# Kernel optimization log

Measured on AMD Instinct MI355X. Metric: run time of the kernel, lower is better.

Reference implementation:

```python
import jax, jax.numpy as jnp
import numpy as np

EPS = 1e-5
GROUPS = 16  # 2*channels // chgn = 128 // 8


def _dft(xr, xi, inverse=False):
    """Matmul-based DFT along the last axis. xi may be None (real input)."""
    N = xr.shape[-1]
    n = jnp.arange(N, dtype=xr.dtype)
    ang = (2.0 * np.pi / N) * (n[:, None] * n[None, :])
    c, s = jnp.cos(ang), jnp.sin(ang)
    if xi is None:
        xi = jnp.zeros_like(xr)
    if inverse:
        yr = (xr @ c - xi @ s) / N
        yi = (xi @ c + xr @ s) / N
    else:
        yr = xr @ c + xi @ s
        yi = xi @ c - xr @ s
    return yr, yi


def _rfft(x):
    w = x.shape[-1]
    yr, yi = _dft(x, None, False)                 # DFT along width
    yr, yi = yr[..., : w // 2 + 1], yi[..., : w // 2 + 1]
    yr, yi = jnp.swapaxes(yr, -1, -2), jnp.swapaxes(yi, -1, -2)
    yr, yi = _dft(yr, yi, False)                  # DFT along height
    return jnp.swapaxes(yr, -1, -2), jnp.swapaxes(yi, -1, -2)


def _irfft(xr, xi):
    yr, yi = jnp.swapaxes(xr, -1, -2), jnp.swapaxes(xi, -1, -2)
    yr, yi = _dft(yr, yi, True)                   # inverse DFT along height
    yr, yi = jnp.swapaxes(yr, -1, -2), jnp.swapaxes(yi, -1, -2)
    # hermitian reconstruction along width
    yr = jnp.concatenate([yr, jnp.flip(yr[..., 1:-1], axis=-1)], axis=-1)
    yi = jnp.concatenate([yi, -jnp.flip(yi[..., 1:-1], axis=-1)], axis=-1)
    yr, _ = _dft(yr, yi, True)                    # inverse DFT along width, keep real
    return yr


def _block(y, conv_w, conv_b, gn_gamma, gn_beta):
    # 1x1 conv
    y = jnp.einsum('bchw,oc->bohw', y, conv_w) + conv_b[None, :, None, None]
    B, C, H, W = y.shape
    yg = y.reshape(B, GROUPS, C // GROUPS, H, W)
    mu = yg.mean(axis=(2, 3, 4), keepdims=True)
    var = yg.var(axis=(2, 3, 4), keepdims=True)
    yg = (yg - mu) * jax.lax.rsqrt(var + EPS)
    y = yg.reshape(B, C, H, W) * gn_gamma[None, :, None, None] + gn_beta[None, :, None, None]
    return jax.nn.relu(y)  # dropout=0.0 -> identity


def _fu(x, conv_w, conv_b, gn_gamma, gn_beta):
    ch = x.shape[1]
    yr, yi = _rfft(x)
    y = jnp.concatenate([yr, yi], axis=1)
    y = _block(y, conv_w, conv_b, gn_gamma, gn_beta)
    return _irfft(y[:, :ch], y[:, ch:])


def setup_inputs() -> dict:
    key = jax.random.key(0)
    k1, k2 = jax.random.split(key)
    x = jax.random.normal(k1, (4, 64, 256, 256), dtype=jnp.float32)
    conv_w = jax.random.normal(k2, (128, 128), dtype=jnp.float32) * (1.0 / np.sqrt(128.0))
    conv_b = jnp.zeros((128,), dtype=jnp.float32)
    gn_gamma = jnp.ones((128,), dtype=jnp.float32)
    gn_beta = jnp.zeros((128,), dtype=jnp.float32)
    return {"x": x, "conv_w": conv_w, "conv_b": conv_b, "gn_gamma": gn_gamma, "gn_beta": gn_beta}


def reference(x, conv_w, conv_b, gn_gamma, gn_beta):
    h = x.shape[2]
    bot = _fu(x[:, :, :-1, :], conv_w, conv_b, gn_gamma, gn_beta)
    top = _fu(x[:, :, 1:, :], conv_w, conv_b, gn_gamma, gn_beta)
    return jnp.concatenate([bot[:, :, : h // 2, :], top[:, :, h // 2 - 1 :, :]], axis=2)
```

## Files before the change

### kernel.cpp

```cpp
#include <hip/hip_runtime.h>
#include <math.h>

#define TPB 256

typedef unsigned short us16;
typedef __bf16 bf16x8 __attribute__((ext_vector_type(8)));
typedef float f32x4 __attribute__((ext_vector_type(4)));

static const int B_ALL = 4;
static const int CH   = 64;
static const int HIN  = 256, WIN = 256;
static const int HH   = 255;
static const int WF   = 129;
static const int HWF  = HH * WF;
static const int SP   = WF * 256;
static const int KH   = 160;
static const int UZ   = 64 * WF;
static const int NBX  = 258;
#define GN_EPS 1e-5f

__device__ __forceinline__ us16 f2bf(float f) {
  union { float f; unsigned u; } v; v.f = f;
  unsigned r = v.u + 0x7FFFu + ((v.u >> 16) & 1u);
  return (us16)(r >> 16);
}
__device__ __forceinline__ float bf2f(us16 v) {
  union { unsigned u; float f; } t; t.u = ((unsigned)v) << 16; return t.f;
}
__device__ __forceinline__ void gload16(const void* g, void* l) {
  __builtin_amdgcn_global_load_lds(
      (const __attribute__((address_space(1))) unsigned int*)g,
      (__attribute__((address_space(3))) unsigned int*)l, 16, 0, 0);
}
#define MFMA __builtin_amdgcn_mfma_f32_16x16x32_bf16
#define WAITVM(N) asm volatile("s_waitcnt vmcnt(" #N ")" ::: "memory")
#define BAR_ACQ() do { \
    __builtin_amdgcn_s_barrier(); \
    asm volatile("" ::: "memory"); \
    __builtin_amdgcn_sched_barrier(0); } while (0)
#define BAR_REL() do { \
    asm volatile("" ::: "memory"); \
    __builtin_amdgcn_s_barrier(); } while (0)

__global__ __launch_bounds__(TPB) void k_zero(float* __restrict__ out, int n) {
  int i = blockIdx.x * TPB + threadIdx.x;
  if (i < n) out[i] = 0.f;
}

__global__ __launch_bounds__(TPB) void k_xcast2(const float* __restrict__ x,
                                                us16* __restrict__ xb,
                                                us16* __restrict__ Frt,
                                                us16* __restrict__ Fit) {
  const int row = blockIdx.x * 4 + (threadIdx.x >> 6);
  const int lane = threadIdx.x & 63;
  float4 v = ((const float4*)(x + (size_t)row * 256))[lane];
  ushort4 o;
  o.x = f2bf(v.x); o.y = f2bf(v.y); o.z = f2bf(v.z); o.w = f2bf(v.w);
  ((ushort4*)(xb + (size_t)row * 256))[lane] = o;
  float alt = v.x - v.y + v.z - v.w;
  for (int off = 32; off; off >>= 1) alt += __shfl_down(alt, off);
  if (lane == 0) {
    int bc = row >> 8, h = row & 255;
    size_t idx = ((size_t)bc * WF + 128) * 256 + h;
    Frt[idx] = f2bf(alt);
    Fit[idx] = 0;
  }
}

__global__ __launch_bounds__(TPB) void k_tables(
    us16* __restrict__ CbA, us16* __restrict__ SbA,
    us16* __restrict__ Tcb, us16* __restrict__ Tsb,
    us16* __restrict__ Tci, us16* __restrict__ Tsi,
    us16* __restrict__ Wpb, us16* __restrict__ Wqb,
    const float* __restrict__ conv_w) {
  int i = blockIdx.x * TPB + threadIdx.x;
  const double PI2 = 6.283185307179586476925286766559;
  if (i < 2 * 65536) {
    int fu = i >> 16, r = (i >> 8) & 255, k = i & 255;
    float cv = 0.f, sv = 0.f;
    int kk = k - fu;
    if (r < 255 && kk >= 0 && kk < 255) {
      double ang = PI2 * (double)((r * kk) % 255) / 255.0;
      cv = (float)cos(ang); sv = (float)sin(ang);
    }
    CbA[i] = f2bf(cv); SbA[i] = f2bf(sv);
  }
  if (i < 128 * 256) {
    int n = i >> 8, w = i & 255;
    double ang = PI2 * (double)((n * w) & 255) / 256.0;
    Tcb[i] = f2bf((float)cos(ang));
    Tsb[i] = f2bf((float)sin(ang));
  }
  if (i < 256 * KH) {
    int w = i / KH, k = i - w * KH;
    float cv = 0.f, sv = 0.f;
    if (k < WF) {
      double coef = (k == 0 || k == 128) ? 1.0 : 2.0;
      double ang = PI2 * (double)((k * w) & 255) / 256.0;
      cv = (float)(coef * cos(ang) / 256.0);
      sv = (float)(coef * sin(ang) / 256.0);
    }
    Tci[i] = f2bf(cv); Tsi[i] = f2bf(sv);
  }
  if (i < 128 * 128) {
    int o = i >> 7, c = i & 127;
    Wpb[i] = f2bf(conv_w[i]);
    float q = (c < 64) ? -conv_w[o * 128 + 64 + c] : conv_w[o * 128 + c - 64];
    Wqb[i] = f2bf(q);
  }
}

__global__ __launch_bounds__(TPB) void k_dftw_fwd_mfma(
    const us16* __restrict__ xb, const us16* __restrict__ Tcb,
    const us16* __restrict__ Tsb, us16* __restrict__ Frt, us16* __restrict__ Fit) {
  __shared__ __align__(16) us16 Ac[2][2][64][32];
  __shared__ __align__(16) us16 As[2][2][64][32];
  __shared__ __align__(16) us16 Bx[2][64][32];
  const int tid = threadIdx.x, w = tid >> 6, lane = tid & 63;
  const int hb = blockIdx.x;
  const int rsel = lane >> 2;
  const int csw = (lane & 3) ^ ((lane >> 3) & 3);
  const us16* gAc = Tcb + (size_t)(16 * w + rsel) * 256 + csw * 8;
  const us16* gAs = Tsb + (size_t)(16 * w + rsel) * 256 + csw * 8;
  const us16* gB  = xb + ((size_t)hb * 64 + 16 * w + rsel) * 256 + csw * 8;
  f32x4 accr[2][4] = {}, acci[2][4] = {};
  const int fr = lane & 15;
  const int kb = 8 * ((lane >> 4) ^ ((lane >> 1) & 3));
#define STAGE_K1(pp, k0) do { \
    gload16(gAc + (k0), &Ac[pp][0][16 * w][0]); \
    gload16(gAc + 64 * 256 + (k0), &Ac[pp][1][16 * w][0]); \
    gload16(gAs + (k0), &As[pp][0][16 * w][0]); \
    gload16(gAs + 64 * 256 + (k0), &As[pp][1][16 * w][0]); \
    gload16(gB + (k0), &Bx[pp][16 * w][0]); } while (0)
  STAGE_K1(0, 0);
  int pp = 0;
  for (int k0 = 0; k0 < 256; k0 += 32) {
    if (k0 + 32 < 256) { STAGE_K1(pp ^ 1, k0 + 32); WAITVM(5); }
    else WAITVM(0);
    BAR_ACQ();
    bf16x8 aC[2], aSn[2];
#pragma unroll
    for (int g = 0; g < 2; ++g) {
      aC[g] = *(const bf16x8*)&Ac[pp][g][16 * w + fr][kb];
      bf16x8 aS = *(const bf16x8*)&As[pp][g][16 * w + fr][kb];
      uint4 su = *(const uint4*)&aS;
      su.x ^= 0x80008000u; su.y ^= 0x80008000u; su.z ^= 0x80008000u; su.w ^= 0x80008000u;
      aSn[g] = *(const bf16x8*)&su;
    }
#pragma unroll
    for (int t = 0; t < 4; ++t) {
      bf16x8 b = *(const bf16x8*)&Bx[pp][16 * t + fr][kb];
#pragma unroll
      for (int g = 0; g < 2; ++g) {
        accr[g][t] = MFMA(aC[g], b, accr[g][t], 0, 0, 0);
        acci[g][t] = MFMA(aSn[g], b, acci[g][t], 0, 0, 0);
      }
    }
    BAR_REL();
    pp ^= 1;
  }
  const int bc = hb >> 2, hl = (hb & 3) * 64;
#pragma unroll
  for (int g = 0; g < 2; ++g) {
#pragma unroll
    for (int t = 0; t < 4; ++t) {
      int h = hl + 16 * t + fr;
#pragma unroll
      for (int j = 0; j < 4; ++j) {
        int n = g * 64 + 16 * w + 4 * (lane >> 4) + j;
        size_t idx = ((size_t)bc * WF + n) * 256 + h;
        Frt[idx] = f2bf(accr[g][t][j]);
        Fit[idx] = f2bf(acci[g][t][j]);
      }
    }
  }
}

__global__ __launch_bounds__(TPB) void k_mix(
    const us16* __restrict__ Frt, const us16* __restrict__ Fit,
    const us16* __restrict__ Wpb, const us16* __restrict__ Wqb,
    us16* __restrict__ P, us16* __restrict__ Q) {
  __shared__ __align__(16) us16 Ap[2][64][32];
  __shared__ __align__(16) us16 Aq[2][64][32];
  __shared__ __align__(8)  us16 Bs[64][36];
  const int tid = threadIdx.x, w = tid >> 6, lane = tid & 63;
  const int sp0 = blockIdx.x * 64, b = blockIdx.z;
  const int rsel = lane >> 2;
  const int csw = (lane & 3) ^ ((lane >> 3) & 3);
  const us16* gAp0 = Wpb + (size_t)(16 * w + rsel) * 128 + csw * 8;
  const us16* gAq0 = Wqb + (size_t)(16 * w + rsel) * 128 + csw * 8;
  f32x4 accp[2][4] = {}, accq[2][4] = {};
  const int fr = lane & 15;
  const int kbA = 8 * ((lane >> 4) ^ ((lane >> 1) & 3));
  const int kbB = 8 * (lane >> 4);
  for (int c0 = 0; c0 < 128; c0 += 32) {
    gload16(gAp0 + c0, &Ap[0][16 * w][0]);
    gload16(gAp0 + 64 * 128 + c0, &Ap[1][16 * w][0]);
    gload16(gAq0 + c0, &Aq[0][16 * w][0]);
    gload16(gAq0 + 64 * 128 + c0, &Aq[1][16 * w][0]);
    for (int f = tid; f < 1024; f += TPB) {
      int cl = f >> 5, spp = f & 31;
      int c = c0 + cl;
      const us16* src = (c < 64) ? Frt : Fit;
      size_t addr = (size_t)(b * 64 + (c & 63)) * SP + sp0 + 2 * spp;
      unsigned v = *(const unsigned*)(src + addr);
      Bs[2 * spp][cl] = (us16)v;
      Bs[2 * spp + 1][cl] = (us16)(v >> 16);
    }
    __syncthreads();
    bf16x8 aP0 = *(const bf16x8*)&Ap[0][16 * w + fr][kbA];
    bf16x8 aP1 = *(const bf16x8*)&Ap[1][16 * w + fr][kbA];
    bf16x8 aQ0 = *(const bf16x8*)&Aq[0][16 * w + fr][kbA];
    bf16x8 aQ1 = *(const bf16x8*)&Aq[1][16 * w + fr][kbA];
#pragma unroll
    for (int t = 0; t < 4; ++t) {
      uint2 lo = *(const uint2*)&Bs[16 * t + fr][kbB];
      uint2 hi = *(const uint2*)&Bs[16 * t + fr][kbB + 4];
      uint4 qq; qq.x = lo.x; qq.y = lo.y; qq.z = hi.x; qq.w = hi.y;
      bf16x8 bb = *(const bf16x8*)&qq;
      accp[0][t] = MFMA(aP0, bb, accp[0][t], 0, 0, 0);
      accp[1][t] = MFMA(aP1, bb, accp[1][t], 0, 0, 0);
      accq[0][t] = MFMA(aQ0, bb, accq[0][t], 0, 0, 0);
      accq[1][t] = MFMA(aQ1, bb, accq[1][t], 0, 0, 0);
    }
    __syncthreads();
  }
#pragma unroll
  for (int t = 0; t < 4; ++t) {
    int sp = sp0 + 16 * t + fr;
#pragma unroll
    for (int ot = 0; ot < 2; ++ot)
#pragma unroll
      for (int j = 0; j < 4; ++j) {
        int o = ot * 64 + 16 * w + 4 * (lane >> 4) + j;
        size_t idx = (size_t)(b * 128 + o) * SP + sp;
        P[idx] = f2bf(accp[ot][t][j]);
        Q[idx] = f2bf(accq[ot][t][j]);
      }
  }
}

__global__ __launch_bounds__(TPB) void k_dfth_fwd2(
    const us16* __restrict__ P, const us16* __restrict__ Q,
    const us16* __restrict__ CbA, const us16* __restrict__ SbA,
    const float* __restrict__ bias, us16* __restrict__ Yt,
    float* __restrict__ gnpart, int fu) {
  __shared__ __align__(16) us16 Ac[2][2][64][32];
  __shared__ __align__(16) us16 As[2][2][64][32];
  __shared__ __align__(16) us16 Bp[2][64][32];
  __shared__ __align__(16) us16 Bq[2][64][32];
  __shared__ float red[4 * TPB];
  const int tid = threadIdx.x, w = tid >> 6, lane = tid & 63;
  const int b = blockIdx.z;
  const int u0 = blockIdx.x * 64;
  const int rsel = lane >> 2;
  const int csw = (lane & 3) ^ ((lane >> 3) & 3);
  const us16* gAc = CbA + (((size_t)fu * 256 + 16 * w + rsel) << 8) + csw * 8;
  const us16* gAs = SbA + (((size_t)fu * 256 + 16 * w + rsel) << 8) + csw * 8;
  const us16* gBp = P + (size_t)b * 128 * SP + (size_t)(u0 + 16 * w + rsel) * 256 + csw * 8;
  const us16* gBq = Q + (size_t)b * 128 * SP + (size_t)(u0 + 16 * w + rsel) * 256 + csw * 8;
  f32x4 cp[2][4] = {}, sq[2][4] = {};
  const int fr = lane & 15;
  const int kb = 8 * ((lane >> 4) ^ ((lane >> 1) & 3));
#define STAGE_K3(pp, k0) do { \
    _Pragma("unroll") \
    for (int mt = 0; mt < 2; ++mt) { \
      gload16(gAc + (mt << 14) + (k0), &Ac[pp][mt][16 * w][0]); \
      gload16(gAs + (mt << 14) + (k0), &As[pp][mt][16 * w][0]); } \
    gload16(gBp + (k0), &Bp[pp][16 * w][0]); \
    gload16(gBq + (k0), &Bq[pp][16 * w][0]); } while (0)
  STAGE_K3(0, 0);
  int pp = 0;
  for (int k0 = 0; k0 < 256; k0 += 32) {
    if (k0 + 32 < 256) { STAGE_K3(pp ^ 1, k0 + 32); WAITVM(6); }
    else WAITVM(0);
    BAR_ACQ();
    bf16x8 aC[2], aS[2];
#pragma unroll
    for (int mt = 0; mt < 2; ++mt) {
      aC[mt] = *(const bf16x8*)&Ac[pp][mt][16 * w + fr][kb];
      aS[mt] = *(const bf16x8*)&As[pp][mt][16 * w + fr][kb];
    }
#pragma unroll
    for (int t = 0; t < 4; ++t) {
      bf16x8 bP = *(const bf16x8*)&Bp[pp][16 * t + fr][kb];
      bf16x8 bQ = *(const bf16x8*)&Bq[pp][16 * t + fr][kb];
#pragma unroll
      for (int mt = 0; mt < 2; ++mt) {
        cp[mt][t] = MFMA(aC[mt], bP, cp[mt][t], 0, 0, 0);
        sq[mt][t] = MFMA(aS[mt], bQ, sq[mt][t], 0, 0, 0);
      }
    }
    BAR_REL();
    pp ^= 1;
  }
  us16* yb = Yt + (size_t)b * 128 * SP;
  const int mb_ = 16 * w + 4 * (lane >> 4);
  const int ub = (u0 / WF + 1) * WF;
  float s0 = 0.f, q0 = 0.f, s1 = 0.f, q1 = 0.f;
#pragma unroll
  for (int t = 0; t < 4; ++t) {
    int u = u0 + 16 * t + fr;
    float bo = bias[u / WF];
    float ts = 0.f, tq = 0.f;
#pragma unroll
    for (int mt = 0; mt < 2; ++mt) {
      int base = mt * 64 + mb_;
      float y[4], z[4];
#pragma unroll
      for (int j = 0; j < 4; ++j) {
        y[j] = cp[mt][t][j] + sq[mt][t][j] + bo;
        z[j] = cp[mt][t][j] - sq[mt][t][j] + bo;
        ts += y[j]; tq += y[j] * y[j];
        if (base + j) { ts += z[j]; tq += z[j] * z[j]; }
      }
      uint2 pk;
      pk.x = (unsigned)f2bf(y[0]) | ((unsigned)f2bf(y[1]) << 16);
      pk.y = (unsigned)f2bf(y[2]) | ((unsigned)f2bf(y[3]) << 16);
      *(uint2*)(yb + (size_t)u * 256 + base) = pk;
      uint2 pk2;
      pk2.x = (unsigned)f2bf(z[3]) | ((unsigned)f2bf(z[2]) << 16);
      pk2.y = (unsigned)f2bf(z[1]) | ((unsigned)f2bf(z[0]) << 16);
      *(uint2*)(yb + (size_t)u * 256 + 252 - base) = pk2;
    }
    if (u >= ub) { s1 += ts; q1 += tq; } else { s0 += ts; q0 += tq; }
  }
  __syncthreads();
  red[tid] = s0; red[TPB + tid] = q0;
  red[2 * TPB + tid] = s1; red[3 * TPB + tid] = q1;
  __syncthreads();
  for (int st = TPB / 2; st > 0; st >>= 1) {
    if (tid < st) {
      red[tid] += red[tid + st];
      red[TPB + tid] += red[TPB + tid + st];
      red[2 * TPB + tid] += red[2 * TPB + tid + st];
      red[3 * TPB + tid] += red[3 * TPB + tid + st];
    }
    __syncthreads();
  }
  if (tid == 0) {
    float* gp = gnpart + ((size_t)b * NBX + blockIdx.x) * 4;
    gp[0] = red[0]; gp[1] = red[TPB];
    gp[2] = red[2 * TPB]; gp[3] = red[3 * TPB];
  }
}

__global__ __launch_bounds__(TPB) void k_gn_stats2(const float* __restrict__ part,
                                                   float* __restrict__ stats) {
  const int bg = blockIdx.x, b = bg >> 4, g = bg & 15;
  const int tid = threadIdx.x;
  const int clo = g * 8, chi = clo + 8;
  float s = 0.f, ss = 0.f;
  for (int bx = tid; bx < NBX; bx += TPB) {
    int c0 = (bx * 64) / WF;
    int c1 = (bx * 64 + 63) / WF;
    const float* p = part + ((size_t)b * NBX + bx) * 4;
    if (c0 >= clo && c0 < chi) { s += p[0]; ss += p[1]; }
    if (c1 != c0 && c1 >= clo && c1 < chi) { s += p[2]; ss += p[3]; }
  }
  __shared__ float rs[TPB], rq[TPB];
  rs[tid] = s; rq[tid] = ss;
  __syncthreads();
  for (int st = TPB / 2; st > 0; st >>= 1) {
    if (tid < st) { rs[tid] += rs[tid + st]; rq[tid] += rq[tid + st]; }
    __syncthreads();
  }
  if (tid == 0) {
    const float inv = 1.f / (8.f * (float)HWF);
    float mean = rs[0] * inv;
    float var = rq[0] * inv - mean * mean;
    stats[bg * 2] = mean;
    stats[bg * 2 + 1] = rsqrtf(var + GN_EPS);
  }
}

__global__ __launch_bounds__(TPB) void k_gnfold(
    const us16* __restrict__ Yt, const float* __restrict__ stats,
    const float* __restrict__ gamma, const float* __restrict__ beta,
    us16* __restrict__ Zrp, us16* __restrict__ Zrm,
    us16* __restrict__ Zip, us16* __restrict__ Zim) {
  const int b = blockIdx.y;
  const int up = blockIdx.x * 8 + (threadIdx.x >> 5);
  const int l32 = threadIdx.x & 31;
  const int c = up / WF;
  const int g1 = b * 16 + (c >> 3), g2 = g1 + 8;
  const float sc1 = gamma[c] * stats[g1 * 2 + 1];
  const float sh1 = beta[c] - stats[g1 * 2] * sc1;
  const float sc2 = gamma[64 + c] * stats[g2 * 2 + 1];
  const float sh2 = beta[64 + c] - stats[g2 * 2] * sc2;
  const us16* ybase = Yt + (size_t)b * 128 * SP;
  const us16* yr = ybase + (size_t)up * 256;
  const us16* yi = ybase + (size_t)(64 * WF + up) * 256;
  const int k0 = l32 * 4;
  uint2 ar = *(const uint2*)(yr + k0);
  uint2 mr = *(const uint2*)(yr + 252 - k0);
  uint2 ai = *(const uint2*)(yi + k0);
  uint2 mi = *(const uint2*)(yi + 252 - k0);
  us16 arv[4] = {(us16)ar.x, (us16)(ar.x >> 16), (us16)ar.y, (us16)(ar.y >> 16)};
  us16 mrv[4] = {(us16)mr.x, (us16)(mr.x >> 16), (us16)mr.y, (us16)(mr.y >> 16)};
  us16 aiv[4] = {(us16)ai.x, (us16)(ai.x >> 16), (us16)ai.y, (us16)(ai.y >> 16)};
  us16 miv[4] = {(us16)mi.x, (us16)(mi.x >> 16), (us16)mi.y, (us16)(mi.y >> 16)};
  us16 rp[4], rm[4], ip[4], im[4];
#pragma unroll
  for (int d = 0; d < 4; ++d) {
    float zr = fmaxf(bf2f(arv[d]) * sc1 + sh1, 0.f);
    float zi = fmaxf(bf2f(aiv[d]) * sc2 + sh2, 0.f);
    float pr = 0.f, pi = 0.f;
    if (k0 + d > 0) {
      pr = fmaxf(bf2f(mrv[3 - d]) * sc1 + sh1, 0.f);
      pi = fmaxf(bf2f(miv[3 - d]) * sc2 + sh2, 0.f);
    }
    rp[d] = f2bf(zr + pr); rm[d] = f2bf(zr - pr);
    ip[d] = f2bf(zi + pi); im[d] = f2bf(zi - pi);
  }
  const size_t zo = ((size_t)b * UZ + up) * 128 + k0;
  uint2 o1; o1.x = (unsigned)rp[0] | ((unsigned)rp[1] << 16);
  o1.y = (unsigned)rp[2] | ((unsigned)rp[3] << 16);
  *(uint2*)(Zrp + zo) = o1;
  uint2 o2; o2.x = (unsigned)rm[0] | ((unsigned)rm[1] << 16);
  o2.y = (unsigned)rm[2] | ((unsigned)rm[3] << 16);
  *(uint2*)(Zrm + zo) = o2;
  uint2 o3; o3.x = (unsigned)ip[0] | ((unsigned)ip[1] << 16);
  o3.y = (unsigned)ip[2] | ((unsigned)ip[3] << 16);
  *(uint2*)(Zip + zo) = o3;
  uint2 o4; o4.x = (unsigned)im[0] | ((unsigned)im[1] << 16);
  o4.y = (unsigned)im[2] | ((unsigned)im[3] << 16);
  *(uint2*)(Zim + zo) = o4;
}

__global__ __launch_bounds__(TPB) void k_dfth_inv_mfma(
    const us16* __restrict__ Zrp, const us16* __restrict__ Zrm,
    const us16* __restrict__ Zip, const us16* __restrict__ Zim,
    const us16* __restrict__ CbA, const us16* __restrict__ SbA,
    us16* __restrict__ Hr, us16* __restrict__ Hi, int hsel) {
  __shared__ __align__(16) us16 Ac[2][2][64][32];
  __shared__ __align__(16) us16 As[2][2][64][32];
  __shared__ __align__(16) us16 Brp[2][64][32];
  __shared__ __align__(16) us16 Brm[2][64][32];
  __shared__ __align__(16) us16 Bip[2][64][32];
  __shared__ __align__(16) us16 Bim[2][64][32];
  const int tid = threadIdx.x, w = tid >> 6, lane = tid & 63;
  const int b = blockIdx.z;
  const int u0 = blockIdx.x * 64;
  const int rsel = lane >> 2;
  const int csw = (lane & 3) ^ ((lane >> 3) & 3);
  const us16* gAc = CbA + (((size_t)hsel + 16 * w + rsel) << 8) + csw * 8;
  const us16* gAs = SbA + (((size_t)hsel + 16 * w + rsel) << 8) + csw * 8;
  const size_t zoff = ((size_t)b * UZ + u0 + 16 * w + rsel) * 128 + csw * 8;
  const us16* gZrp = Zrp + zoff;
  const us16* gZrm = Zrm + zoff;
  const us16* gZip = Zip + zoff;
  const us16* gZim = Zim + zoff;
  f32x4 accr[2][4] = {}, acci[2][4] = {};
  const int fr = lane & 15;
  const int kb = 8 * ((lane >> 4) ^ ((lane >> 1) & 3));
#define STAGE_K6(pp, k0) do { \
    gload16(gAc + (k0), &Ac[pp][0][16 * w][0]); \
    gload16(gAc + (1 << 14) + (k0), &Ac[pp][1][16 * w][0]); \
    gload16(gAs + (k0), &As[pp][0][16 * w][0]); \
    gload16(gAs + (1 << 14) + (k0), &As[pp][1][16 * w][0]); \
    gload16(gZrp + (k0), &Brp[pp][16 * w][0]); \
    gload16(gZrm + (k0), &Brm[pp][16 * w][0]); \
    gload16(gZip + (k0), &Bip[pp][16 * w][0]); \
    gload16(gZim + (k0), &Bim[pp][16 * w][0]); } while (0)
  STAGE_K6(0, 0);
  int pp = 0;
  for (int k0 = 0; k0 < 128; k0 += 32) {
    if (k0 + 32 < 128) { STAGE_K6(pp ^ 1, k0 + 32); WAITVM(8); }
    else WAITVM(0);
    BAR_ACQ();
    bf16x8 aC[2], aS[2], aSn[2];
#pragma unroll
    for (int mt = 0; mt < 2; ++mt) {
      aC[mt] = *(const bf16x8*)&Ac[pp][mt][16 * w + fr][kb];
      aS[mt] = *(const bf16x8*)&As[pp][mt][16 * w + fr][kb];
      uint4 su = *(const uint4*)&aS[mt];
      su.x ^= 0x80008000u; su.y ^= 0x80008000u; su.z ^= 0x80008000u; su.w ^= 0x80008000u;
      aSn[mt] = *(const bf16x8*)&su;
    }
#pragma unroll
    for (int t = 0; t < 4; ++t) {
      bf16x8 bRp = *(const bf16x8*)&Brp[pp][16 * t + fr][kb];
      bf16x8 bRm = *(const bf16x8*)&Brm[pp][16 * t + fr][kb];
      bf16x8 bIp = *(const bf16x8*)&Bip[pp][16 * t + fr][kb];
      bf16x8 bIm = *(const bf16x8*)&Bim[pp][16 * t + fr][kb];
#pragma unroll
      for (int mt = 0; mt < 2; ++mt) {
        accr[mt][t] = MFMA(aC[mt], bRp, accr[mt][t], 0, 0, 0);
        accr[mt][t] = MFMA(aSn[mt], bIm, accr[mt][t], 0, 0, 0);
        acci[mt][t] = MFMA(aC[mt], bIp, acci[mt][t], 0, 0, 0);
        acci[mt][t] = MFMA(aS[mt], bRm, acci[mt][t], 0, 0, 0);
      }
    }
    BAR_REL();
    pp ^= 1;
  }
  const float inv = 1.f / 255.f;
#pragma unroll
  for (int t = 0; t < 4; ++t) {
    int u = u0 + 16 * t + fr;
    int c = u / WF, n = u - c * WF;
#pragma unroll
    for (int mt = 0; mt < 2; ++mt) {
#pragma unroll
      for (int j = 0; j < 4; ++j) {
        int m = mt * 64 + 16 * w + 4 * (lane >> 4) + j;
        size_t idx = (((size_t)(b * 64 + c)) * 128 + m) * KH + n;
        Hr[idx] = f2bf(accr[mt][t][j] * inv);
        Hi[idx] = f2bf(acci[mt][t][j] * inv);
      }
    }
  }
}

__global__ __launch_bounds__(TPB) void k_dftw_inv_mfma(
    const us16* __restrict__ Hr, const us16* __restrict__ Hi,
    const us16* __restrict__ Tci, const us16* __restrict__ Tsi,
    float* __restrict__ out, int roff, int b0) {
  __shared__ __align__(16) us16 Ar[2][64][32];
  __shared__ __align__(16) us16 Ai[2][64][32];
  __shared__ __align__(16) us16 Bc[2][64][32];
  __shared__ __align__(16) us16 Bs[2][64][32];
  const int tid = threadIdx.x, w = tid >> 6, lane = tid & 63;
  const int w0 = blockIdx.x * 64, mf0 = blockIdx.y * 64;
  const int rsel = lane >> 2;
  const int csw = (lane & 3) ^ ((lane >> 3) & 3);
  const us16* gAr = Hr + (size_t)(mf0 + 16 * w + rsel) * KH + csw * 8;
  const us16* gAi = Hi + (size_t)(mf0 + 16 * w + rsel) * KH + csw * 8;
  const us16* gBc = Tci + (size_t)(w0 + 16 * w + rsel) * KH + csw * 8;
  const us16* gBs = Tsi + (size_t)(w0 + 16 * w + rsel) * KH + csw * 8;
  f32x4 accU[4] = {}, accV[4] = {};
  const int fr = lane & 15;
  const int kb = 8 * ((lane >> 4) ^ ((lane >> 1) & 3));
#define STAGE_K7(pp, k0) do { \
    gload16(gAr + (k0), &Ar[pp][16 * w][0]); \
    gload16(gAi + (k0), &Ai[pp][16 * w][0]); \
    gload16(gBc + (k0), &Bc[pp][16 * w][0]); \
    gload16(gBs + (k0), &Bs[pp][16 * w][0]); } while (0)
  STAGE_K7(0, 0);
  int pp = 0;
  for (int k0 = 0; k0 < KH; k0 += 32) {
    if (k0 + 32 < KH) { STAGE_K7(pp ^ 1, k0 + 32); WAITVM(4); }
    else WAITVM(0);
    BAR_ACQ();
    bf16x8 aR = *(const bf16x8*)&Ar[pp][16 * w + fr][kb];
    bf16x8 aI = *(const bf16x8*)&Ai[pp][16 * w + fr][kb];
    uint4 su = *(const uint4*)&aI;
    su.x ^= 0x80008000u; su.y ^= 0x80008000u; su.z ^= 0x80008000u; su.w ^= 0x80008000u;
    bf16x8 aIn = *(const bf16x8*)&su;
#pragma unroll
    for (int t = 0; t < 4; ++t) {
      bf16x8 bC = *(const bf16x8*)&Bc[pp][16 * t + fr][kb];
      bf16x8 bS = *(const bf16x8*)&Bs[pp][16 * t + fr][kb];
      accU[t] = MFMA(aR, bC, accU[t], 0, 0, 0);
      accV[t] = MFMA(aIn, bS, accV[t], 0, 0, 0);
    }
    BAR_REL();
    pp ^= 1;
  }
#pragma unroll
  for (int t = 0; t < 4; ++t) {
    int wv = w0 + 16 * t + fr;
#pragma unroll
    for (int j = 0; j < 4; ++j) {
      int mf = mf0 + 16 * w + 4 * (lane >> 4) + j;
      int bcl = mf >> 7, mrow = mf & 127;
      int bb = b0 + (bcl >> 6), cc = bcl & 63;
      size_t obase = (((size_t)bb * CH + cc) * HIN + roff + mrow) * WIN;
      float U = accU[t][j], V = accV[t][j];
      out[obase + wv] = U + V;
      if (wv > 0) out[obase + 256 - wv] = U - V;
    }
  }
}

__global__ __launch_bounds__(TPB) void k_w128(const us16* __restrict__ Hr,
                                              float* __restrict__ out,
                                              int roff, int b0) {
  const int mf = blockIdx.x * TPB + threadIdx.x;
  const us16* hr = Hr + (size_t)mf * KH;
  float s = bf2f(hr[0]) + bf2f(hr[128]);
  for (int k = 1; k < 128; k += 2)
    s += -2.f * bf2f(hr[k]) + 2.f * bf2f(hr[k + 1]);
  s -= 2.f * bf2f(hr[128]);
  s *= (1.f / 256.f);
  int bcl = mf >> 7, mrow = mf & 127;
  int bb = b0 + (bcl >> 6), cc = bcl & 63;
  out[(((size_t)bb * CH + cc) * HIN + roff + mrow) * WIN + 128] = s;
}

extern "C" void kernel_launch(void* const* d_in, const int* in_sizes, int n_in,
                              void* d_out, int out_size, void* d_ws, size_t ws_size,
                              hipStream_t stream) {
  const float* x        = (const float*)d_in[0];
  const float* conv_w   = (const float*)d_in[1];
  const float* conv_b   = (const float*)d_in[2];
  const float* gn_gamma = (const float*)d_in[3];
  const float* gn_beta  = (const float*)d_in[4];
  float* out = (float*)d_out;

  const size_t uCbA = 2 * 65536;
  const size_t uTcb = 128 * 256;
  const size_t uTci = (size_t)256 * KH;
  const size_t uW   = 128 * 128;
  const size_t fixed_u16 = 2 * uCbA + 2 * uTcb + 2 * uTci + 2 * uW;
  const size_t uXB = (size_t)CH * HIN * WIN;
  const size_t uF  = (size_t)CH * SP;
  const size_t uPQ = (size_t)128 * SP;
  const size_t uYT = (size_t)128 * SP;
  const size_t uH  = (size_t)CH * 128 * KH;
  const size_t uZ1 = (size_t)UZ * 128;
  const size_t per_u16 = uXB + 2 * uF + 2 * uPQ + 4 * uZ1;
  const size_t nPart = 4 * 4 * NBX + 128;

  int nb = 0;
  for (int cand = 4; cand >= 1; cand >>= 1) {
    size_t need = fixed_u16 * 2 + nPart * 4 + (size_t)cand * per_u16 * 2 + 256;
    if (need <= ws_size) { nb = cand; break; }
  }
  if (nb == 0) {
    k_zero<<<dim3((out_size + TPB - 1) / TPB), dim3(TPB), 0, stream>>>(out, out_size);
    return;
  }

  us16* CbA = (us16*)d_ws;
  us16* SbA = CbA + uCbA;
  us16* Tcb = SbA + uCbA;
  us16* Tsb = Tcb + uTcb;
  us16* Tci = Tsb + uTcb;
  us16* Tsi = Tci + uTci;
  us16* Wpb = Tsi + uTci;
  us16* Wqb = Wpb + uW;
  float* part  = (float*)(Wqb + uW);
  float* stats = part + 4 * NBX * 4;
  us16* xb  = (us16*)(stats + 128);
  us16* Frt = xb + (size_t)nb * uXB;
  us16* Fit = Frt + (size_t)nb * uF;
  us16* P   = Fit + (size_t)nb * uF;
  us16* Q   = P + (size_t)nb * uPQ;
  us16* Zrp = Q + (size_t)nb * uPQ;
  us16* Zrm = Zrp + (size_t)nb * uZ1;
  us16* Zip = Zrm + (size_t)nb * uZ1;
  us16* Zim = Zip + (size_t)nb * uZ1;
  us16* Yt  = xb;
  us16* Hr  = xb + (size_t)nb * uYT;
  us16* Hi  = Hr + (size_t)nb * uH;

  k_tables<<<dim3(512), dim3(TPB), 0, stream>>>(CbA, SbA, Tcb, Tsb, Tci, Tsi,
                                                Wpb, Wqb, conv_w);

  for (int b0 = 0; b0 < B_ALL; b0 += nb) {
    k_xcast2<<<dim3(nb * 4096), dim3(TPB), 0, stream>>>(
        x + (size_t)b0 * CH * HIN * WIN, xb, Frt, Fit);
    k_dftw_fwd_mfma<<<dim3(nb * 256), dim3(TPB), 0, stream>>>(
        xb, Tcb, Tsb, Frt, Fit);
    k_mix<<<dim3(SP / 64, 1, nb), dim3(TPB), 0, stream>>>(
        Frt, Fit, Wpb, Wqb, P, Q);
    for (int fu = 0; fu < 2; ++fu) {
      const int hsel = fu ? 127 : 0;
      const int roff = fu ? 128 : 0;
      k_dfth_fwd2<<<dim3(NBX, 1, nb), dim3(TPB), 0, stream>>>(
          P, Q, CbA, SbA, conv_b, Yt, part, fu);
      k_gn_stats2<<<dim3(nb * 16), dim3(TPB), 0, stream>>>(part, stats);
      k_gnfold<<<dim3(UZ / 8, nb), dim3(TPB), 0, stream>>>(
          Yt, stats, gn_gamma, gn_beta, Zrp, Zrm, Zip, Zim);
      k_dfth_inv_mfma<<<dim3(UZ / 64, 1, nb), dim3(TPB), 0, stream>>>(
          Zrp, Zrm, Zip, Zim, CbA, SbA, Hr, Hi, hsel);
      k_dftw_inv_mfma<<<dim3(2, nb * 128), dim3(TPB), 0, stream>>>(
          Hr, Hi, Tci, Tsi, out, roff, b0);
      k_w128<<<dim3(nb * 32), dim3(TPB), 0, stream>>>(Hr, out, roff, b0);
    }
  }
}
```

Measured before the change: 248.8 us.

## Compute both shifted-window forward height DFTs in one kernel via phase rotation

The two forward height-DFT launches (one per shifted window) are merged into one kernel. The second window's result comes from the first window's DFT sums by a per-frequency twiddle rotation plus a boundary-row correction, so the P/Q inputs and the DFT tables are read once instead of twice. In exchange the kernel runs twice as many MFMAs per tile (four accumulator sets instead of two), uses more registers, and writes both outputs, which needs an extra Yt buffer and duplicated GN partial sums. The rotation identity also changes rounding relative to computing the second window directly.

Result: slower. 260.1 us (+4.6%).

```diff
diff --git a/kernel.cpp b/kernel.cpp
--- a/kernel.cpp
+++ b/kernel.cpp
@@ -72,6 +72,7 @@
     us16* __restrict__ Tcb, us16* __restrict__ Tsb,
     us16* __restrict__ Tci, us16* __restrict__ Tsi,
     us16* __restrict__ Wpb, us16* __restrict__ Wqb,
+    float* __restrict__ rot,
     const float* __restrict__ conv_w) {
   int i = blockIdx.x * TPB + threadIdx.x;
   const double PI2 = 6.283185307179586476925286766559;
@@ -107,6 +108,11 @@
     Wpb[i] = f2bf(conv_w[i]);
     float q = (c < 64) ? -conv_w[o * 128 + 64 + c] : conv_w[o * 128 + c - 64];
     Wqb[i] = f2bf(q);
+  }
+  if (i < 128) {
+    double ang = PI2 * (double)i / 255.0;
+    rot[2 * i] = (float)cos(ang);
+    rot[2 * i + 1] = (float)sin(ang);
   }
 }
 
@@ -243,23 +249,23 @@
 __global__ __launch_bounds__(TPB) void k_dfth_fwd2(
     const us16* __restrict__ P, const us16* __restrict__ Q,
     const us16* __restrict__ CbA, const us16* __restrict__ SbA,
-    const float* __restrict__ bias, us16* __restrict__ Yt,
-    float* __restrict__ gnpart, int fu) {
+    const float* __restrict__ bias, const float* __restrict__ rot,
+    us16* __restrict__ Yt0, us16* __restrict__ Yt1,
+    float* __restrict__ gnpart) {
   __shared__ __align__(16) us16 Ac[2][2][64][32];
   __shared__ __align__(16) us16 As[2][2][64][32];
   __shared__ __align__(16) us16 Bp[2][64][32];
   __shared__ __align__(16) us16 Bq[2][64][32];
-  __shared__ float red[4 * TPB];
   const int tid = threadIdx.x, w = tid >> 6, lane = tid & 63;
   const int b = blockIdx.z;
   const int u0 = blockIdx.x * 64;
   const int rsel = lane >> 2;
   const int csw = (lane & 3) ^ ((lane >> 3) & 3);
-  const us16* gAc = CbA + (((size_t)fu * 256 + 16 * w + rsel) << 8) + csw * 8;
-  const us16* gAs = SbA + (((size_t)fu * 256 + 16 * w + rsel) << 8) + csw * 8;
+  const us16* gAc = CbA + (((size_t)(16 * w + rsel)) << 8) + csw * 8;
+  const us16* gAs = SbA + (((size_t)(16 * w + rsel)) << 8) + csw * 8;
   const us16* gBp = P + (size_t)b * 128 * SP + (size_t)(u0 + 16 * w + rsel) * 256 + csw * 8;
   const us16* gBq = Q + (size_t)b * 128 * SP + (size_t)(u0 + 16 * w + rsel) * 256 + csw * 8;
-  f32x4 cp[2][4] = {}, sq[2][4] = {};
+  f32x4 cp[2][4] = {}, sq[2][4] = {}, sp_[2][4] = {}, cq[2][4] = {};
   const int fr = lane & 15;
   const int kb = 8 * ((lane >> 4) ^ ((lane >> 1) & 3));
 #define STAGE_K3(pp, k0) do { \
@@ -287,61 +293,98 @@
       bf16x8 bQ = *(const bf16x8*)&Bq[pp][16 * t + fr][kb];
 #pragma unroll
       for (int mt = 0; mt < 2; ++mt) {
-        cp[mt][t] = MFMA(aC[mt], bP, cp[mt][t], 0, 0, 0);
-        sq[mt][t] = MFMA(aS[mt], bQ, sq[mt][t], 0, 0, 0);
+        cp[mt][t]  = MFMA(aC[mt], bP, cp[mt][t], 0, 0, 0);
+        sp_[mt][t] = MFMA(aS[mt], bP, sp_[mt][t], 0, 0, 0);
+        cq[mt][t]  = MFMA(aC[mt], bQ, cq[mt][t], 0, 0, 0);
+        sq[mt][t]  = MFMA(aS[mt], bQ, sq[mt][t], 0, 0, 0);
       }
     }
     BAR_REL();
     pp ^= 1;
   }
-  us16* yb = Yt + (size_t)b * 128 * SP;
+  us16* yb0 = Yt0 + (size_t)b * 128 * SP;
+  us16* yb1 = Yt1 + (size_t)b * 128 * SP;
+  const us16* pb = P + (size_t)b * 128 * SP;
+  const us16* qb = Q + (size_t)b * 128 * SP;
   const int mb_ = 16 * w + 4 * (lane >> 4);
   const int ub = (u0 / WF + 1) * WF;
-  float s0 = 0.f, q0 = 0.f, s1 = 0.f, q1 = 0.f;
+  float rc[2][4], rs[2][4];
+#pragma unroll
+  for (int mt = 0; mt < 2; ++mt)
+#pragma unroll
+    for (int j = 0; j < 4; ++j) {
+      int r = mt * 64 + mb_ + j;
+      rc[mt][j] = rot[2 * r];
+      rs[mt][j] = rot[2 * r + 1];
+    }
+  float s0f0 = 0.f, q0f0 = 0.f, s1f0 = 0.f, q1f0 = 0.f;
+  float s0f1 = 0.f, q0f1 = 0.f, s1f1 = 0.f, q1f1 = 0.f;
 #pragma unroll
   for (int t = 0; t < 4; ++t) {
     int u = u0 + 16 * t + fr;
     float bo = bias[u / WF];
-    float ts = 0.f, tq = 0.f;
+    float dP = bf2f(pb[(size_t)u * 256 + 255]) - bf2f(pb[(size_t)u * 256]);
+    float dQ = bf2f(qb[(size_t)u * 256 + 255]) - bf2f(qb[(size_t)u * 256]);
+    float t0s = 0.f, t0q = 0.f, t1s = 0.f, t1q = 0.f;
 #pragma unroll
     for (int mt = 0; mt < 2; ++mt) {
       int base = mt * 64 + mb_;
-      float y[4], z[4];
+      float y0[4], z0[4], y1[4], z1[4];
 #pragma unroll
       for (int j = 0; j < 4; ++j) {
-        y[j] = cp[mt][t][j] + sq[mt][t][j] + bo;
-        z[j] = cp[mt][t][j] - sq[mt][t][j] + bo;
-        ts += y[j]; tq += y[j] * y[j];
-        if (base + j) { ts += z[j]; tq += z[j] * z[j]; }
+        float CPv = cp[mt][t][j], SQv = sq[mt][t][j];
+        float SPv = sp_[mt][t][j], CQv = cq[mt][t][j];
+        y0[j] = CPv + SQv + bo;
+        z0[j] = CPv - SQv + bo;
+        float E1 = rc[mt][j] * (CPv + dP) + rs[mt][j] * SPv;
+        float O1 = rc[mt][j] * SQv - rs[mt][j] * (CQv + dQ);
+        y1[j] = E1 + O1 + bo;
+        z1[j] = E1 - O1 + bo;
+        t0s += y0[j]; t0q += y0[j] * y0[j];
+        t1s += y1[j]; t1q += y1[j] * y1[j];
+        if (base + j) {
+          t0s += z0[j]; t0q += z0[j] * z0[j];
+          t1s += z1[j]; t1q += z1[j] * z1[j];
+        }
       }
       uint2 pk;
-      pk.x = (unsigned)f2bf(y[0]) | ((unsigned)f2bf(y[1]) << 16);
-      pk.y = (unsigned)f2bf(y[2]) | ((unsigned)f2bf(y[3]) << 16);
-      *(uint2*)(yb + (size_t)u * 256 + base) = pk;
-      uint2 pk2;
-      pk2.x = (unsigned)f2bf(z[3]) | ((unsigned)f2bf(z[2]) << 16);
-      pk2.y = (unsigned)f2bf(z[1]) | ((unsigned)f2bf(z[0]) << 16);
-      *(uint2*)(yb + (size_t)u * 256 + 252 - base) = pk2;
-    }
-    if (u >= ub) { s1 += ts; q1 += tq; } else { s0 += ts; q0 += tq; }
-  }
+      pk.x = (unsigned)f2bf(y0[0]) | ((unsigned)f2bf(y0[1]) << 16);
+      pk.y = (unsigned)f2bf(y0[2]) | ((unsigned)f2bf(y0[3]) << 16);
+      *(uint2*)(yb0 + (size_t)u * 256 + base) = pk;
+      pk.x = (unsigned)f2bf(z0[3]) | ((unsigned)f2bf(z0[2]) << 16);
+      pk.y = (unsigned)f2bf(z0[1]) | ((unsigned)f2bf(z0[0]) << 16);
+      *(uint2*)(yb0 + (size_t)u * 256 + 252 - base) = pk;
+      pk.x = (unsigned)f2bf(y1[0]) | ((unsigned)f2bf(y1[1]) << 16);
+      pk.y = (unsigned)f2bf(y1[2]) | ((unsigned)f2bf(y1[3]) << 16);
+      *(uint2*)(yb1 + (size_t)u * 256 + base) = pk;
+      pk.x = (unsigned)f2bf(z1[3]) | ((unsigned)f2bf(z1[2]) << 16);
+      pk.y = (unsigned)f2bf(z1[1]) | ((unsigned)f2bf(z1[0]) << 16);
+      *(uint2*)(yb1 + (size_t)u * 256 + 252 - base) = pk;
+    }
+    if (u >= ub) { s1f0 += t0s; q1f0 += t0q; s1f1 += t1s; q1f1 += t1q; }
+    else { s0f0 += t0s; q0f0 += t0q; s0f1 += t1s; q0f1 += t1q; }
+  }
+  float* red = (float*)&Ac[0][0][0][0];
   __syncthreads();
-  red[tid] = s0; red[TPB + tid] = q0;
-  red[2 * TPB + tid] = s1; red[3 * TPB + tid] = q1;
+  red[tid] = s0f0; red[TPB + tid] = q0f0;
+  red[2 * TPB + tid] = s1f0; red[3 * TPB + tid] = q1f0;
+  red[4 * TPB + tid] = s0f1; red[5 * TPB + tid] = q0f1;
+  red[6 * TPB + tid] = s1f1; red[7 * TPB + tid] = q1f1;
   __syncthreads();
   for (int st = TPB / 2; st > 0; st >>= 1) {
     if (tid < st) {
-      red[tid] += red[tid + st];
-      red[TPB + tid] += red[TPB + tid + st];
-      red[2 * TPB + tid] += red[2 * TPB + tid + st];
-      red[3 * TPB + tid] += red[3 * TPB + tid + st];
+#pragma unroll
+      for (int k = 0; k < 8; ++k) red[k * TPB + tid] += red[k * TPB + tid + st];
     }
     __syncthreads();
   }
   if (tid == 0) {
-    float* gp = gnpart + ((size_t)b * NBX + blockIdx.x) * 4;
-    gp[0] = red[0]; gp[1] = red[TPB];
-    gp[2] = red[2 * TPB]; gp[3] = red[3 * TPB];
+    float* gp0 = gnpart + ((size_t)b * NBX + blockIdx.x) * 4;
+    float* gp1 = gnpart + (((size_t)gridDim.z + b) * NBX + blockIdx.x) * 4;
+    gp0[0] = red[0]; gp0[1] = red[TPB];
+    gp0[2] = red[2 * TPB]; gp0[3] = red[3 * TPB];
+    gp1[0] = red[4 * TPB]; gp1[1] = red[5 * TPB];
+    gp1[2] = red[6 * TPB]; gp1[3] = red[7 * TPB];
   }
 }
 
@@ -610,8 +653,8 @@
   const size_t uYT = (size_t)128 * SP;
   const size_t uH  = (size_t)CH * 128 * KH;
   const size_t uZ1 = (size_t)UZ * 128;
-  const size_t per_u16 = uXB + 2 * uF + 2 * uPQ + 4 * uZ1;
-  const size_t nPart = 4 * 4 * NBX + 128;
+  const size_t per_u16 = uXB + 2 * uF + 2 * uPQ + 4 * uZ1 + uYT;
+  const size_t nPart = 2 * 4 * NBX * 4 + 256 + 256;
 
   int nb = 0;
   for (int cand = 4; cand >= 1; cand >>= 1) {
@@ -632,8 +675,9 @@
   us16* Wpb = Tsi + uTci;
   us16* Wqb = Wpb + uW;
   float* part  = (float*)(Wqb + uW);
-  float* stats = part + 4 * NBX * 4;
-  us16* xb  = (us16*)(stats + 128);
+  float* stats = part + 2 * 4 * NBX * 4;
+  float* rot   = stats + 256;
+  us16* xb  = (us16*)(rot + 256);
   us16* Frt = xb + (size_t)nb * uXB;
   us16* Fit = Frt + (size_t)nb * uF;
   us16* P   = Fit + (size_t)nb * uF;
@@ -642,12 +686,13 @@
   us16* Zrm = Zrp + (size_t)nb * uZ1;
   us16* Zip = Zrm + (size_t)nb * uZ1;
   us16* Zim = Zip + (size_t)nb * uZ1;
-  us16* Yt  = xb;
+  us16* Yt1 = Zim + (size_t)nb * uZ1;
+  us16* Yt0 = xb;
   us16* Hr  = xb + (size_t)nb * uYT;
   us16* Hi  = Hr + (size_t)nb * uH;
 
   k_tables<<<dim3(512), dim3(TPB), 0, stream>>>(CbA, SbA, Tcb, Tsb, Tci, Tsi,
-                                                Wpb, Wqb, conv_w);
+                                                Wpb, Wqb, rot, conv_w);
 
   for (int b0 = 0; b0 < B_ALL; b0 += nb) {
     k_xcast2<<<dim3(nb * 4096), dim3(TPB), 0, stream>>>(
@@ -656,14 +701,17 @@
         xb, Tcb, Tsb, Frt, Fit);
     k_mix<<<dim3(SP / 64, 1, nb), dim3(TPB), 0, stream>>>(
         Frt, Fit, Wpb, Wqb, P, Q);
+    k_dfth_fwd2<<<dim3(NBX, 1, nb), dim3(TPB), 0, stream>>>(
+        P, Q, CbA, SbA, conv_b, rot, Yt0, Yt1, part);
     for (int fu = 0; fu < 2; ++fu) {
       const int hsel = fu ? 127 : 0;
       const int roff = fu ? 128 : 0;
-      k_dfth_fwd2<<<dim3(NBX, 1, nb), dim3(TPB), 0, stream>>>(
-          P, Q, CbA, SbA, conv_b, Yt, part, fu);
-      k_gn_stats2<<<dim3(nb * 16), dim3(TPB), 0, stream>>>(part, stats);
+      const us16* Yt = fu ? Yt1 : Yt0;
+      float* pfu = part + (size_t)fu * nb * NBX * 4;
+      float* sfu = stats + (size_t)fu * nb * 32;
+      k_gn_stats2<<<dim3(nb * 16), dim3(TPB), 0, stream>>>(pfu, sfu);
       k_gnfold<<<dim3(UZ / 8, nb), dim3(TPB), 0, stream>>>(
-          Yt, stats, gn_gamma, gn_beta, Zrp, Zrm, Zip, Zim);
+          Yt, sfu, gn_gamma, gn_beta, Zrp, Zrm, Zip, Zim);
       k_dfth_inv_mfma<<<dim3(UZ / 64, 1, nb), dim3(TPB), 0, stream>>>(
           Zrp, Zrm, Zip, Zim, CbA, SbA, Hr, Hi, hsel);
       k_dftw_inv_mfma<<<dim3(2, nb * 128), dim3(TPB), 0, stream>>>(
```

## Batch both FU halves into single launches via grid dimension

Applied to the files above, without the earlier changes.

Replaces the per-half loop (fu=0,1) with single launches of each post-mix kernel, using a grid dimension to select the half. Buffers for Yt, Hr/Hi, GN partials and stats are duplicated per half, and the Z buffers are re-aliased onto the P/Q region. This halves the kernel launch count and doubles the grid size per launch, which improves occupancy and cuts launch gaps. The cost is a larger workspace footprint, which may force a smaller batch chunk nb if the workspace is tight. Aliasing Z onto P/Q is safe only because the forward DFT-H kernel fully consumes P/Q before gnfold writes Z.

Result: faster. 224.4 us (-9.8%).

```diff
diff --git a/kernel.cpp b/kernel.cpp
--- a/kernel.cpp
+++ b/kernel.cpp
@@ -243,14 +243,15 @@
 __global__ __launch_bounds__(TPB) void k_dfth_fwd2(
     const us16* __restrict__ P, const us16* __restrict__ Q,
     const us16* __restrict__ CbA, const us16* __restrict__ SbA,
-    const float* __restrict__ bias, us16* __restrict__ Yt,
-    float* __restrict__ gnpart, int fu) {
+    const float* __restrict__ bias, us16* __restrict__ Yt0,
+    us16* __restrict__ Yt1, float* __restrict__ gnpart) {
   __shared__ __align__(16) us16 Ac[2][2][64][32];
   __shared__ __align__(16) us16 As[2][2][64][32];
   __shared__ __align__(16) us16 Bp[2][64][32];
   __shared__ __align__(16) us16 Bq[2][64][32];
   __shared__ float red[4 * TPB];
   const int tid = threadIdx.x, w = tid >> 6, lane = tid & 63;
+  const int fu = blockIdx.y;
   const int b = blockIdx.z;
   const int u0 = blockIdx.x * 64;
   const int rsel = lane >> 2;
@@ -294,7 +295,7 @@
     BAR_REL();
     pp ^= 1;
   }
-  us16* yb = Yt + (size_t)b * 128 * SP;
+  us16* yb = (fu ? Yt1 : Yt0) + (size_t)b * 128 * SP;
   const int mb_ = 16 * w + 4 * (lane >> 4);
   const int ub = (u0 / WF + 1) * WF;
   float s0 = 0.f, q0 = 0.f, s1 = 0.f, q1 = 0.f;
@@ -339,7 +340,7 @@
     __syncthreads();
   }
   if (tid == 0) {
-    float* gp = gnpart + ((size_t)b * NBX + blockIdx.x) * 4;
+    float* gp = gnpart + ((((size_t)fu * gridDim.z) + b) * NBX + blockIdx.x) * 4;
     gp[0] = red[0]; gp[1] = red[TPB];
     gp[2] = red[2 * TPB]; gp[3] = red[3 * TPB];
   }
@@ -348,13 +349,16 @@
 __global__ __launch_bounds__(TPB) void k_gn_stats2(const float* __restrict__ part,
                                                    float* __restrict__ stats) {
   const int bg = blockIdx.x, b = bg >> 4, g = bg & 15;
+  const int fu = blockIdx.y;
+  const int nbv = gridDim.x >> 4;
+  const float* pbase = part + (size_t)fu * nbv * NBX * 4;
   const int tid = threadIdx.x;
   const int clo = g * 8, chi = clo + 8;
   float s = 0.f, ss = 0.f;
   for (int bx = tid; bx < NBX; bx += TPB) {
     int c0 = (bx * 64) / WF;
     int c1 = (bx * 64 + 63) / WF;
-    const float* p = part + ((size_t)b * NBX + bx) * 4;
+    const float* p = pbase + ((size_t)b * NBX + bx) * 4;
     if (c0 >= clo && c0 < chi) { s += p[0]; ss += p[1]; }
     if (c1 != c0 && c1 >= clo && c1 < chi) { s += p[2]; ss += p[3]; }
   }
@@ -369,26 +373,31 @@
     const float inv = 1.f / (8.f * (float)HWF);
     float mean = rs[0] * inv;
     float var = rq[0] * inv - mean * mean;
-    stats[bg * 2] = mean;
-    stats[bg * 2 + 1] = rsqrtf(var + GN_EPS);
+    float* sb = stats + (size_t)fu * nbv * 32;
+    sb[bg * 2] = mean;
+    sb[bg * 2 + 1] = rsqrtf(var + GN_EPS);
   }
 }
 
 __global__ __launch_bounds__(TPB) void k_gnfold(
-    const us16* __restrict__ Yt, const float* __restrict__ stats,
+    const us16* __restrict__ Yt0, const us16* __restrict__ Yt1,
+    const float* __restrict__ stats,
     const float* __restrict__ gamma, const float* __restrict__ beta,
     us16* __restrict__ Zrp, us16* __restrict__ Zrm,
     us16* __restrict__ Zip, us16* __restrict__ Zim) {
   const int b = blockIdx.y;
+  const int fu = blockIdx.z;
+  const int nbv = gridDim.y;
   const int up = blockIdx.x * 8 + (threadIdx.x >> 5);
   const int l32 = threadIdx.x & 31;
   const int c = up / WF;
+  const float* sb = stats + (size_t)fu * nbv * 32;
   const int g1 = b * 16 + (c >> 3), g2 = g1 + 8;
-  const float sc1 = gamma[c] * stats[g1 * 2 + 1];
-  const float sh1 = beta[c] - stats[g1 * 2] * sc1;
-  const float sc2 = gamma[64 + c] * stats[g2 * 2 + 1];
-  const float sh2 = beta[64 + c] - stats[g2 * 2] * sc2;
-  const us16* ybase = Yt + (size_t)b * 128 * SP;
+  const float sc1 = gamma[c] * sb[g1 * 2 + 1];
+  const float sh1 = beta[c] - sb[g1 * 2] * sc1;
+  const float sc2 = gamma[64 + c] * sb[g2 * 2 + 1];
+  const float sh2 = beta[64 + c] - sb[g2 * 2] * sc2;
+  const us16* ybase = (fu ? Yt1 : Yt0) + (size_t)b * 128 * SP;
   const us16* yr = ybase + (size_t)up * 256;
   const us16* yi = ybase + (size_t)(64 * WF + up) * 256;
   const int k0 = l32 * 4;
@@ -413,7 +422,7 @@
     rp[d] = f2bf(zr + pr); rm[d] = f2bf(zr - pr);
     ip[d] = f2bf(zi + pi); im[d] = f2bf(zi - pi);
   }
-  const size_t zo = ((size_t)b * UZ + up) * 128 + k0;
+  const size_t zo = (((size_t)fu * nbv + b) * UZ + up) * 128 + k0;
   uint2 o1; o1.x = (unsigned)rp[0] | ((unsigned)rp[1] << 16);
   o1.y = (unsigned)rp[2] | ((unsigned)rp[3] << 16);
   *(uint2*)(Zrp + zo) = o1;
@@ -432,7 +441,8 @@
     const us16* __restrict__ Zrp, const us16* __restrict__ Zrm,
     const us16* __restrict__ Zip, const us16* __restrict__ Zim,
     const us16* __restrict__ CbA, const us16* __restrict__ SbA,
-    us16* __restrict__ Hr, us16* __restrict__ Hi, int hsel) {
+    us16* __restrict__ Hr0, us16* __restrict__ Hi0,
+    us16* __restrict__ Hr1, us16* __restrict__ Hi1) {
   __shared__ __align__(16) us16 Ac[2][2][64][32];
   __shared__ __align__(16) us16 As[2][2][64][32];
   __shared__ __align__(16) us16 Brp[2][64][32];
@@ -440,13 +450,16 @@
   __shared__ __align__(16) us16 Bip[2][64][32];
   __shared__ __align__(16) us16 Bim[2][64][32];
   const int tid = threadIdx.x, w = tid >> 6, lane = tid & 63;
+  const int fu = blockIdx.y;
   const int b = blockIdx.z;
+  const int nbv = gridDim.z;
+  const int hsel = fu ? 127 : 0;
   const int u0 = blockIdx.x * 64;
   const int rsel = lane >> 2;
   const int csw = (lane & 3) ^ ((lane >> 3) & 3);
   const us16* gAc = CbA + (((size_t)hsel + 16 * w + rsel) << 8) + csw * 8;
   const us16* gAs = SbA + (((size_t)hsel + 16 * w + rsel) << 8) + csw * 8;
-  const size_t zoff = ((size_t)b * UZ + u0 + 16 * w + rsel) * 128 + csw * 8;
+  const size_t zoff = (((size_t)fu * nbv + b) * UZ + u0 + 16 * w + rsel) * 128 + csw * 8;
   const us16* gZrp = Zrp + zoff;
   const us16* gZrm = Zrm + zoff;
   const us16* gZip = Zip + zoff;
@@ -495,6 +508,8 @@
     BAR_REL();
     pp ^= 1;
   }
+  us16* Hr = fu ? Hr1 : Hr0;
+  us16* Hi = fu ? Hi1 : Hi0;
   const float inv = 1.f / 255.f;
 #pragma unroll
   for (int t = 0; t < 4; ++t) {
@@ -514,15 +529,20 @@
 }
 
 __global__ __launch_bounds__(TPB) void k_dftw_inv_mfma(
-    const us16* __restrict__ Hr, const us16* __restrict__ Hi,
+    const us16* __restrict__ Hr0, const us16* __restrict__ Hi0,
+    const us16* __restrict__ Hr1, const us16* __restrict__ Hi1,
     const us16* __restrict__ Tci, const us16* __restrict__ Tsi,
-    float* __restrict__ out, int roff, int b0) {
+    float* __restrict__ out, int b0) {
   __shared__ __align__(16) us16 Ar[2][64][32];
   __shared__ __align__(16) us16 Ai[2][64][32];
   __shared__ __align__(16) us16 Bc[2][64][32];
   __shared__ __align__(16) us16 Bs[2][64][32];
   const int tid = threadIdx.x, w = tid >> 6, lane = tid & 63;
   const int w0 = blockIdx.x * 64, mf0 = blockIdx.y * 64;
+  const int fu = blockIdx.z;
+  const int roff = fu << 7;
+  const us16* Hr = fu ? Hr1 : Hr0;
+  const us16* Hi = fu ? Hi1 : Hi0;
   const int rsel = lane >> 2;
   const int csw = (lane & 3) ^ ((lane >> 3) & 3);
   const us16* gAr = Hr + (size_t)(mf0 + 16 * w + rsel) * KH + csw * 8;
@@ -574,11 +594,13 @@
   }
 }
 
-__global__ __launch_bounds__(TPB) void k_w128(const us16* __restrict__ Hr,
-                                              float* __restrict__ out,
-                                              int roff, int b0) {
+__global__ __launch_bounds__(TPB) void k_w128(const us16* __restrict__ Hr0,
+                                              const us16* __restrict__ Hr1,
+                                              float* __restrict__ out, int b0) {
   const int mf = blockIdx.x * TPB + threadIdx.x;
-  const us16* hr = Hr + (size_t)mf * KH;
+  const int fu = blockIdx.y;
+  const int roff = fu << 7;
+  const us16* hr = (fu ? Hr1 : Hr0) + (size_t)mf * KH;
   float s = bf2f(hr[0]) + bf2f(hr[128]);
   for (int k = 1; k < 128; k += 2)
     s += -2.f * bf2f(hr[k]) + 2.f * bf2f(hr[k + 1]);
@@ -610,8 +632,8 @@
   const size_t uYT = (size_t)128 * SP;
   const size_t uH  = (size_t)CH * 128 * KH;
   const size_t uZ1 = (size_t)UZ * 128;
-  const size_t per_u16 = uXB + 2 * uF + 2 * uPQ + 4 * uZ1;
-  const size_t nPart = 4 * 4 * NBX + 128;
+  const size_t per_u16 = uXB + 2 * uF + 2 * uPQ + uYT + 2 * uH;
+  const size_t nPart = 2 * 4 * NBX * 4 + 256;
 
   int nb = 0;
   for (int cand = 4; cand >= 1; cand >>= 1) {
@@ -632,19 +654,22 @@
   us16* Wpb = Tsi + uTci;
   us16* Wqb = Wpb + uW;
   float* part  = (float*)(Wqb + uW);
-  float* stats = part + 4 * NBX * 4;
-  us16* xb  = (us16*)(stats + 128);
+  float* stats = part + 2 * 4 * NBX * 4;
+  us16* xb  = (us16*)(stats + 256);
   us16* Frt = xb + (size_t)nb * uXB;
   us16* Fit = Frt + (size_t)nb * uF;
   us16* P   = Fit + (size_t)nb * uF;
   us16* Q   = P + (size_t)nb * uPQ;
-  us16* Zrp = Q + (size_t)nb * uPQ;
-  us16* Zrm = Zrp + (size_t)nb * uZ1;
-  us16* Zip = Zrm + (size_t)nb * uZ1;
-  us16* Zim = Zip + (size_t)nb * uZ1;
-  us16* Yt  = xb;
-  us16* Hr  = xb + (size_t)nb * uYT;
-  us16* Hi  = Hr + (size_t)nb * uH;
+  us16* Yt1 = Q + (size_t)nb * uPQ;
+  us16* Hr1 = Yt1 + (size_t)nb * uYT;
+  us16* Hi1 = Hr1 + (size_t)nb * uH;
+  us16* Zrp = P;
+  us16* Zrm = Zrp + 2 * (size_t)nb * uZ1;
+  us16* Zip = Zrm + 2 * (size_t)nb * uZ1;
+  us16* Zim = Zip + 2 * (size_t)nb * uZ1;
+  us16* Yt0 = xb;
+  us16* Hr0 = xb + (size_t)nb * uYT;
+  us16* Hi0 = Hr0 + (size_t)nb * uH;
 
   k_tables<<<dim3(512), dim3(TPB), 0, stream>>>(CbA, SbA, Tcb, Tsb, Tci, Tsi,
                                                 Wpb, Wqb, conv_w);
@@ -656,19 +681,15 @@
         xb, Tcb, Tsb, Frt, Fit);
     k_mix<<<dim3(SP / 64, 1, nb), dim3(TPB), 0, stream>>>(
         Frt, Fit, Wpb, Wqb, P, Q);
-    for (int fu = 0; fu < 2; ++fu) {
-      const int hsel = fu ? 127 : 0;
-      const int roff = fu ? 128 : 0;
-      k_dfth_fwd2<<<dim3(NBX, 1, nb), dim3(TPB), 0, stream>>>(
-          P, Q, CbA, SbA, conv_b, Yt, part, fu);
-      k_gn_stats2<<<dim3(nb * 16), dim3(TPB), 0, stream>>>(part, stats);
-      k_gnfold<<<dim3(UZ / 8, nb), dim3(TPB), 0, stream>>>(
-          Yt, stats, gn_gamma, gn_beta, Zrp, Zrm, Zip, Zim);
-      k_dfth_inv_mfma<<<dim3(UZ / 64, 1, nb), dim3(TPB), 0, stream>>>(
-          Zrp, Zrm, Zip, Zim, CbA, SbA, Hr, Hi, hsel);
-      k_dftw_inv_mfma<<<dim3(2, nb * 128), dim3(TPB), 0, stream>>>(
-          Hr, Hi, Tci, Tsi, out, roff, b0);
-      k_w128<<<dim3(nb * 32), dim3(TPB), 0, stream>>>(Hr, out, roff, b0);
-    }
-  }
-}
+    k_dfth_fwd2<<<dim3(NBX, 2, nb), dim3(TPB), 0, stream>>>(
+        P, Q, CbA, SbA, conv_b, Yt0, Yt1, part);
+    k_gn_stats2<<<dim3(nb * 16, 2), dim3(TPB), 0, stream>>>(part, stats);
+    k_gnfold<<<dim3(UZ / 8, nb, 2), dim3(TPB), 0, stream>>>(
+        Yt0, Yt1, stats, gn_gamma, gn_beta, Zrp, Zrm, Zip, Zim);
+    k_dfth_inv_mfma<<<dim3(UZ / 64, 2, nb), dim3(TPB), 0, stream>>>(
+        Zrp, Zrm, Zip, Zim, CbA, SbA, Hr0, Hi0, Hr1, Hi1);
+    k_dftw_inv_mfma<<<dim3(2, nb * 128, 2), dim3(TPB), 0, stream>>>(
+        Hr0, Hi0, Hr1, Hi1, Tci, Tsi, out, b0);
+    k_w128<<<dim3(nb * 32, 2), dim3(TPB), 0, stream>>>(Hr0, Hr1, out, b0);
+  }
+}
```
